# Optimization experiments

Hardware: AMD Instinct MI355X
Metric: run time of the kernel (lower is better)

## Reference

```python
import jax, jax.numpy as jnp
import numpy as np

N, E, D, G = 100000, 600000, 128, 256  # nodes, edges, feat dim, num graphs
EPS = 1e-5


def graph_norm(x, batch, weight, bias, mean_scale):
    # PyG GraphNorm: per-graph mean/var with learnable mean_scale
    counts = jax.ops.segment_sum(jnp.ones((x.shape[0],), x.dtype), batch, num_segments=G)
    counts = jnp.maximum(counts, 1.0)[:, None]  # [G,1]
    mean = jax.ops.segment_sum(x, batch, num_segments=G) / counts  # [G,D]
    out = x - mean[batch] * mean_scale  # [N,D]
    var = jax.ops.segment_sum(out * out, batch, num_segments=G) / counts  # [G,D]
    inv_std = jax.lax.rsqrt(var + EPS)[batch]  # [N,D]
    return weight * out * inv_std + bias


def sage_conv_max(x, edge_index, w_l, b_l, w_r):
    # SAGEConv(aggr='max'): gather x[src], scatter-max into dst, then two linears
    src, dst = edge_index[0], edge_index[1]
    agg = jax.ops.segment_max(x[src], dst, num_segments=N)  # [N,D], -inf for empty
    agg = jnp.where(jnp.isfinite(agg), agg, 0.0)  # PyG fills empty segments with 0
    return agg @ w_l.T + b_l + x @ w_r.T


def setup_inputs() -> dict:
    key = jax.random.key(0)
    ks = jax.random.split(key, 6)
    x = jax.random.normal(ks[0], (N, D), dtype=jnp.float32)
    edge_index = jax.random.randint(ks[1], (2, E), 0, N, dtype=jnp.int64)
    batch = jnp.sort(jax.random.randint(ks[2], (N,), 0, G, dtype=jnp.int64))
    s = 1.0 / np.sqrt(D)
    return {
        "x": x,
        "edge_index": edge_index,
        "batch": batch,
        "n1_w": jnp.ones((D,), jnp.float32),
        "n1_b": jnp.zeros((D,), jnp.float32),
        "n1_ms": jnp.ones((D,), jnp.float32),
        "n2_w": jnp.ones((D,), jnp.float32),
        "n2_b": jnp.zeros((D,), jnp.float32),
        "n2_ms": jnp.ones((D,), jnp.float32),
        "w_l": jax.random.uniform(ks[3], (D, D), jnp.float32, -s, s),
        "b_l": jax.random.uniform(ks[4], (D,), jnp.float32, -s, s),
        "w_r": jax.random.uniform(ks[5], (D, D), jnp.float32, -s, s),
    }


def reference(x, edge_index, batch, n1_w, n1_b, n1_ms, n2_w, n2_b, n2_ms, w_l, b_l, w_r):
    h = graph_norm(x, batch, n1_w, n1_b, n1_ms)
    h = sage_conv_max(h, edge_index, w_l, b_l, w_r)
    h = jax.nn.relu(x + h)
    h = graph_norm(h, batch, n2_w, n2_b, n2_ms)
    return h
```

## Files before the change

kernel.cpp:

```cpp
#include <hip/hip_runtime.h>
#include <math.h>

#define NN 100000
#define EE 600000
#define DD 128
#define GG 256
#define EPSV 1e-5f

typedef __attribute__((ext_vector_type(8))) __bf16 bf16x8;
typedef __attribute__((ext_vector_type(16))) float f32x16;
typedef __attribute__((ext_vector_type(4))) unsigned short us4;

#define OFF_A1      0
#define OFF_B1      131072
#define OFF_A2      262144
#define OFF_B2      393216
#define OFF_DEG     524288
#define OFF_ROWPTR  924288
#define OFF_CURSOR  1324352
#define OFF_BSUMS   1724352
#define OFF_CNT     1726400
#define OFF_ELIST   1728448
#define OFF_WB      4128448
#define OFF_H1B     4193984
#define WS_NEED_A   (OFF_H1B + 25600000ULL)

#define NB_STATS 782
#define NB_EDGE  2344
#define NB_H1B   12500
#define NB1024   98

__device__ __forceinline__ int lower_bound_i(const int* __restrict__ a, int n, int v) {
    int lo = 0, hi = n;
    while (lo < hi) { int mid = (lo + hi) >> 1; if (a[mid] < v) lo = mid + 1; else hi = mid; }
    return lo;
}

__device__ __forceinline__ unsigned short f2bf(float f) {
    unsigned int u = __float_as_uint(f);
    unsigned int r = u + 0x7fffu + ((u >> 16) & 1u);
    return (unsigned short)(r >> 16);
}

__device__ __forceinline__ void stats_body(
    const float* __restrict__ X, const int* __restrict__ batch,
    float* __restrict__ Sg, float* __restrict__ Qg, int blk)
{
    int t = threadIdx.x;
    int rl = t >> 5, fq = t & 31;
    int r0 = blk * 128;
    int rend = r0 + 128; if (rend > NN) rend = NN;
    __shared__ float ls[8 * 128];
    __shared__ float lq[8 * 128];
    int g0 = batch[r0], g1 = batch[rend - 1];
    const float4* X4 = (const float4*)X;
    for (int g = g0; g <= g1; ++g) {
        int sa = (g == g0) ? r0   : lower_bound_i(batch, NN, g);
        int sb = (g == g1) ? rend : lower_bound_i(batch, NN, g + 1);
        float s0 = 0.f, s1 = 0.f, s2 = 0.f, s3 = 0.f;
        float q0 = 0.f, q1 = 0.f, q2 = 0.f, q3 = 0.f;
        for (int r = sa + rl; r < sb; r += 8) {
            float4 v = X4[r * 32 + fq];
            s0 += v.x; s1 += v.y; s2 += v.z; s3 += v.w;
            q0 += v.x * v.x; q1 += v.y * v.y; q2 += v.z * v.z; q3 += v.w * v.w;
        }
        ls[rl * 128 + fq * 4 + 0] = s0; ls[rl * 128 + fq * 4 + 1] = s1;
        ls[rl * 128 + fq * 4 + 2] = s2; ls[rl * 128 + fq * 4 + 3] = s3;
        lq[rl * 128 + fq * 4 + 0] = q0; lq[rl * 128 + fq * 4 + 1] = q1;
        lq[rl * 128 + fq * 4 + 2] = q2; lq[rl * 128 + fq * 4 + 3] = q3;
        __syncthreads();
        if (t < 32) {
            #pragma unroll
            for (int k = 0; k < 4; k++) {
                float as = 0.f, aq = 0.f;
                #pragma unroll
                for (int j = 0; j < 8; j++) { as += ls[j * 128 + t * 4 + k]; aq += lq[j * 128 + t * 4 + k]; }
                atomicAdd(&Sg[g * DD + t * 4 + k], as);
                atomicAdd(&Qg[g * DD + t * 4 + k], aq);
            }
        }
        __syncthreads();
    }
}

__global__ __launch_bounds__(256) void stats_p1(
    const float* __restrict__ X, const int* __restrict__ batch,
    float* __restrict__ Sg, float* __restrict__ Qg)
{
    stats_body(X, batch, Sg, Qg, blockIdx.x);
}

__global__ __launch_bounds__(256) void statsdeg_kernel(
    const float* __restrict__ X, const int* __restrict__ batch,
    float* __restrict__ Sg, float* __restrict__ Qg,
    const int* __restrict__ dst, int* __restrict__ deg)
{
    int b = blockIdx.x;
    if (b < NB_STATS) { stats_body(X, batch, Sg, Qg, b); return; }
    int e = (b - NB_STATS) * 256 + threadIdx.x;
    if (e < EE) atomicAdd(&deg[dst[e]], 1);
}

__global__ __launch_bounds__(128) void finalize_kernel(
    const int* __restrict__ batch, float* S, float* Q,
    const float* __restrict__ w, const float* __restrict__ bb, const float* __restrict__ ms,
    unsigned short* __restrict__ wb, const float* __restrict__ wl, const float* __restrict__ wr,
    int* __restrict__ cnt, int doW)
{
    int g = blockIdx.x;
    if (g >= GG) {
        if (!doW) return;
        const float* W = (g == GG) ? wl : wr;
        int kofs = (g == GG) ? 0 : 128;
        for (int tt = threadIdx.x; tt < DD * 32; tt += 128) {
            int j = tt >> 5, k4 = tt & 31;
            float4 v = ((const float4*)W)[j * 32 + k4];
            us4 o = { f2bf(v.x), f2bf(v.y), f2bf(v.z), f2bf(v.w) };
            *(us4*)&wb[j * 256 + kofs + k4 * 4] = o;
        }
        return;
    }
    __shared__ int sh[2];
    if (threadIdx.x == 0) { sh[0] = lower_bound_i(batch, NN, g); sh[1] = lower_bound_i(batch, NN, g + 1); }
    __syncthreads();
    int c_n = sh[1] - sh[0];
    if (cnt && threadIdx.x == 0) cnt[g] = c_n;
    float c = (float)(c_n > 0 ? c_n : 1);
    float inv_c = 1.0f / c;
    int d = threadIdx.x;
    float m  = S[g * DD + d] * inv_c;
    float qm = Q[g * DD + d] * inv_c;
    float sc = ms[d];
    float var = qm - m * m * sc * (2.0f - sc);
    float Ad = w[d] * rsqrtf(var + EPSV);
    S[g * DD + d] = Ad;
    Q[g * DD + d] = bb[d] - Ad * m * sc;
}

__global__ __launch_bounds__(256) void h1bscan_kernel(
    const float* __restrict__ X, const int* __restrict__ batch,
    const float* __restrict__ A1, const float* __restrict__ B1, unsigned short* __restrict__ h1b,
    const int* __restrict__ deg, int* __restrict__ bsums)
{
    int blk = blockIdx.x;
    if (blk < NB_H1B) {
        int f = blk * 256 + threadIdx.x;
        int i = f >> 5, c = f & 31;
        int g = batch[i];
        float4 v = ((const float4*)X)[f];
        float4 a = ((const float4*)A1)[g * 32 + c];
        float4 b = ((const float4*)B1)[g * 32 + c];
        us4 o = { f2bf(fmaf(a.x, v.x, b.x)), f2bf(fmaf(a.y, v.y, b.y)),
                  f2bf(fmaf(a.z, v.z, b.z)), f2bf(fmaf(a.w, v.w, b.w)) };
        *(us4*)&h1b[i * DD + c * 4] = o;
        return;
    }
    int b = blk - NB_H1B, t = threadIdx.x;
    int base = b * 1024 + t * 4;
    int v = 0;
    #pragma unroll
    for (int k = 0; k < 4; k++) { int i = base + k; if (i < NN) v += deg[i]; }
    __shared__ int sd[256];
    sd[t] = v; __syncthreads();
    for (int off = 128; off > 0; off >>= 1) { if (t < off) sd[t] += sd[t + off]; __syncthreads(); }
    if (t == 0) bsums[b] = sd[0];
}

__global__ __launch_bounds__(256) void scan1(const int* __restrict__ deg, int* __restrict__ bsums) {
    int b = blockIdx.x, t = threadIdx.x;
    int base = b * 1024 + t * 4;
    int v = 0;
    #pragma unroll
    for (int k = 0; k < 4; k++) { int i = base + k; if (i < NN) v += deg[i]; }
    __shared__ int sd[256];
    sd[t] = v; __syncthreads();
    for (int off = 128; off > 0; off >>= 1) { if (t < off) sd[t] += sd[t + off]; __syncthreads(); }
    if (t == 0) bsums[b] = sd[0];
}

__global__ __launch_bounds__(256) void scan3(const int* __restrict__ deg, const int* __restrict__ bsums,
                                             int* __restrict__ rowptr, int* __restrict__ cursor) {
    int b = blockIdx.x, t = threadIdx.x;
    int boff = 0;
    for (int j = 0; j < b; j++) boff += bsums[j];
    int base = b * 1024 + t * 4;
    int d0 = 0, d1 = 0, d2 = 0, d3 = 0;
    if (base     < NN) d0 = deg[base];
    if (base + 1 < NN) d1 = deg[base + 1];
    if (base + 2 < NN) d2 = deg[base + 2];
    if (base + 3 < NN) d3 = deg[base + 3];
    int tsum = d0 + d1 + d2 + d3;
    __shared__ int sd[256];
    sd[t] = tsum; __syncthreads();
    for (int off = 1; off < 256; off <<= 1) {
        int a = (t >= off) ? sd[t - off] : 0;
        __syncthreads();
        sd[t] += a;
        __syncthreads();
    }
    int exc = sd[t] - tsum + boff;
    int p0 = exc, p1 = exc + d0, p2 = exc + d0 + d1, p3 = exc + d0 + d1 + d2;
    if (base     < NN) { rowptr[base]     = p0; cursor[base]     = p0; }
    if (base + 1 < NN) { rowptr[base + 1] = p1; cursor[base + 1] = p1; }
    if (base + 2 < NN) { rowptr[base + 2] = p2; cursor[base + 2] = p2; }
    if (base + 3 < NN) { rowptr[base + 3] = p3; cursor[base + 3] = p3; }
    if (b == 0 && t == 0) rowptr[NN] = EE;
}

__global__ __launch_bounds__(256) void fill_kernel(const int* __restrict__ src, const int* __restrict__ dst,
                                                   int* __restrict__ cursor, int* __restrict__ elist) {
    int e = blockIdx.x * 256 + threadIdx.x;
    if (e < EE) {
        int p = atomicAdd(&cursor[dst[e]], 1);
        elist[p] = src[e];
    }
}

#define USTR 264
__global__ __launch_bounds__(512) void gemm_mega(
    const float* __restrict__ X, const unsigned short* __restrict__ h1b,
    const int* __restrict__ batch, const int* __restrict__ rowptr, const int* __restrict__ elist,
    const unsigned short* __restrict__ wb, const float* __restrict__ blv,
    float* __restrict__ Sg2, float* __restrict__ Qg2, float* __restrict__ out)
{
    __shared__ unsigned short sU[64 * USTR];
    __shared__ int sBatch[64];
    int tid = threadIdx.x;
    int i0 = blockIdx.x * 64;
    int lane = tid & 63, wave = tid >> 6;
    int m = lane & 31, hf = lane >> 5;

    for (int t = tid; t < 64 * 16; t += 512) {
        int r = t >> 4, c = t & 15;
        int i = i0 + r; if (i >= NN) i = NN - 1;
        uint4 v = ((const uint4*)(h1b + (size_t)i * DD))[c];
        *(uint4*)&sU[r * USTR + 128 + c * 8] = v;
    }
    if (tid < 64) {
        int i = i0 + tid;
        sBatch[tid] = (i < NN) ? batch[i] : -1;
    }

    int hw = tid >> 5, j = tid & 31;
    for (int rr = hw; rr < 64; rr += 16) {
        int i = i0 + rr;
        int beg = 0, end = 0;
        if (i < NN) { beg = rowptr[i]; end = rowptr[i + 1]; }
        float a0 = -INFINITY, a1 = -INFINITY, a2 = -INFINITY, a3 = -INFINITY;
        int last = end - 1;
        for (int e = beg; e < end; e += 8) {
            int n[8];
            #pragma unroll
            for (int k = 0; k < 8; k++) { int t2 = e + k; n[k] = elist[t2 < last ? t2 : last]; }
            us4 p[8];
            #pragma unroll
            for (int k = 0; k < 8; k++) p[k] = *(const us4*)(h1b + (size_t)n[k] * DD + j * 4);
            #pragma unroll
            for (int k = 0; k < 8; k++) {
                a0 = fmaxf(a0, __uint_as_float((unsigned)p[k][0] << 16));
                a1 = fmaxf(a1, __uint_as_float((unsigned)p[k][1] << 16));
                a2 = fmaxf(a2, __uint_as_float((unsigned)p[k][2] << 16));
                a3 = fmaxf(a3, __uint_as_float((unsigned)p[k][3] << 16));
            }
        }
        us4 r4 = { 0, 0, 0, 0 };
        if (end > beg) {
            r4[0] = (unsigned short)(__float_as_uint(a0) >> 16);
            r4[1] = (unsigned short)(__float_as_uint(a1) >> 16);
            r4[2] = (unsigned short)(__float_as_uint(a2) >> 16);
            r4[3] = (unsigned short)(__float_as_uint(a3) >> 16);
        }
        *(us4*)&sU[rr * USTR + j * 4] = r4;
    }
    __syncthreads();

    int rbase = (wave >> 2) * 32;
    int col = (wave & 3) * 32 + m;
    const unsigned short* bcol = wb + col * 256 + hf * 8;
    const unsigned short* arow = &sU[(rbase + m) * USTR + hf * 8];

    f32x16 acc;
    #pragma unroll
    for (int r = 0; r < 16; r++) acc[r] = 0.f;
    #pragma unroll
    for (int s = 0; s < 16; s++) {
        bf16x8 b = *(const bf16x8*)(bcol + s * 16);
        bf16x8 a = *(const bf16x8*)(arow + s * 16);
        acc = __builtin_amdgcn_mfma_f32_32x32x16_bf16(a, b, acc, 0, 0, 0);
    }

    float blc = blv[col];
    float s_run = 0.f, q_run = 0.f;
    int cur_g = -1;
    #pragma unroll
    for (int reg = 0; reg < 16; reg++) {
        int rl = (reg & 3) + 8 * (reg >> 2) + 4 * hf;
        int i = i0 + rbase + rl;
        if (i < NN) {
            float v = X[i * DD + col] + blc + acc[reg];
            v = v > 0.f ? v : 0.f;
            out[i * DD + col] = v;
            int g = sBatch[rbase + rl];
            if (g != cur_g) {
                if (cur_g >= 0) {
                    atomicAdd(&Sg2[cur_g * DD + col], s_run);
                    atomicAdd(&Qg2[cur_g * DD + col], q_run);
                }
                cur_g = g; s_run = 0.f; q_run = 0.f;
            }
            s_run += v; q_run += v * v;
        }
    }
    if (cur_g >= 0) {
        atomicAdd(&Sg2[cur_g * DD + col], s_run);
        atomicAdd(&Qg2[cur_g * DD + col], q_run);
    }
}

__global__ __launch_bounds__(256) void apply_a(
    float* __restrict__ H, const int* __restrict__ batch,
    const float* __restrict__ Sg2, const float* __restrict__ Qg2, const int* __restrict__ cnt,
    const float* __restrict__ w2, const float* __restrict__ b2, const float* __restrict__ ms2)
{
    int f = blockIdx.x * 256 + threadIdx.x;
    if (f >= NN * 32) return;
    int i = f >> 5, c = f & 31;
    int g = batch[i];
    int cg = cnt[g];
    float invc = 1.0f / (float)(cg > 0 ? cg : 1);
    float4 S  = ((const float4*)Sg2)[g * 32 + c];
    float4 Q  = ((const float4*)Qg2)[g * 32 + c];
    float4 W  = ((const float4*)w2)[c];
    float4 Bv = ((const float4*)b2)[c];
    float4 Ms = ((const float4*)ms2)[c];
    float4 v = ((float4*)H)[f];
    {
        float mm = S.x * invc, qm = Q.x * invc;
        float A = W.x * rsqrtf(qm - mm * mm * Ms.x * (2.0f - Ms.x) + EPSV);
        v.x = fmaf(A, v.x, Bv.x - A * mm * Ms.x);
    }
    {
        float mm = S.y * invc, qm = Q.y * invc;
        float A = W.y * rsqrtf(qm - mm * mm * Ms.y * (2.0f - Ms.y) + EPSV);
        v.y = fmaf(A, v.y, Bv.y - A * mm * Ms.y);
    }
    {
        float mm = S.z * invc, qm = Q.z * invc;
        float A = W.z * rsqrtf(qm - mm * mm * Ms.z * (2.0f - Ms.z) + EPSV);
        v.z = fmaf(A, v.z, Bv.z - A * mm * Ms.z);
    }
    {
        float mm = S.w * invc, qm = Q.w * invc;
        float A = W.w * rsqrtf(qm - mm * mm * Ms.w * (2.0f - Ms.w) + EPSV);
        v.w = fmaf(A, v.w, Bv.w - A * mm * Ms.w);
    }
    ((float4*)H)[f] = v;
}

__global__ __launch_bounds__(256) void apply_b(float* __restrict__ H, const int* __restrict__ batch,
                                               const float* __restrict__ A2, const float* __restrict__ B2) {
    int f = blockIdx.x * 256 + threadIdx.x;
    if (f >= NN * 32) return;
    int i = f >> 5, c = f & 31;
    int g = batch[i];
    float4 v = ((float4*)H)[f];
    float4 a = ((const float4*)A2)[g * 32 + c];
    float4 b = ((const float4*)B2)[g * 32 + c];
    v.x = fmaf(a.x, v.x, b.x); v.y = fmaf(a.y, v.y, b.y);
    v.z = fmaf(a.z, v.z, b.z); v.w = fmaf(a.w, v.w, b.w);
    ((float4*)H)[f] = v;
}

__global__ __launch_bounds__(256) void agg_b(
    const float* __restrict__ X, const int* __restrict__ batch,
    const float* __restrict__ A1, const float* __restrict__ B1,
    const int* __restrict__ rowptr, const int* __restrict__ elist, float* __restrict__ H)
{
    int i = blockIdx.x * 2 + (threadIdx.x >> 7);
    int d = threadIdx.x & 127;
    int beg = rowptr[i], end = rowptr[i + 1];
    float acc = -INFINITY;
    int e = beg;
    for (; e + 2 <= end; e += 2) {
        int s0 = elist[e], s1 = elist[e + 1];
        int g0 = batch[s0], g1 = batch[s1];
        float v0 = fmaf(A1[g0 * DD + d], X[s0 * DD + d], B1[g0 * DD + d]);
        float v1 = fmaf(A1[g1 * DD + d], X[s1 * DD + d], B1[g1 * DD + d]);
        acc = fmaxf(acc, fmaxf(v0, v1));
    }
    for (; e < end; e++) {
        int s = elist[e]; int g = batch[s];
        acc = fmaxf(acc, fmaf(A1[g * DD + d], X[s * DD + d], B1[g * DD + d]));
    }
    if (end == beg) acc = 0.f;
    H[i * DD + d] = acc;
}

#define BM 128
#define LDT 72
__global__ __launch_bounds__(256) void gemm_b(
    const float* __restrict__ X, const int* __restrict__ batch,
    const float* __restrict__ A1, const float* __restrict__ B1,
    const float* __restrict__ wl, const float* __restrict__ blv, const float* __restrict__ wr,
    float* __restrict__ H)
{
    __shared__ unsigned short Ut[BM * LDT];
    __shared__ unsigned short Wt[DD * LDT];
    int i0 = blockIdx.x * BM;
    int tid = threadIdx.x;
    int lane = tid & 63, wave = tid >> 6;
    int wrow = (wave >> 1) * 64, wcol = (wave & 1) * 64;
    int m = lane & 31, hf = lane >> 5;

    f32x16 acc00, acc01, acc10, acc11;
    #pragma unroll
    for (int r = 0; r < 16; r++) { acc00[r] = 0.f; acc01[r] = 0.f; acc10[r] = 0.f; acc11[r] = 0.f; }

    for (int c = 0; c < 4; c++) {
        __syncthreads();
        for (int t = tid; t < BM * 16; t += 256) {
            int r = t >> 4, c4 = t & 15;
            int i = i0 + r; if (i >= NN) i = NN - 1;
            float4 v;
            if (c < 2) {
                v = ((const float4*)H)[i * 32 + c * 16 + c4];
            } else {
                int g = batch[i];
                float4 xv = ((const float4*)X)[i * 32 + (c - 2) * 16 + c4];
                float4 a = ((const float4*)A1)[g * 32 + (c - 2) * 16 + c4];
                float4 b = ((const float4*)B1)[g * 32 + (c - 2) * 16 + c4];
                v.x = fmaf(a.x, xv.x, b.x); v.y = fmaf(a.y, xv.y, b.y);
                v.z = fmaf(a.z, xv.z, b.z); v.w = fmaf(a.w, xv.w, b.w);
            }
            us4 o = { f2bf(v.x), f2bf(v.y), f2bf(v.z), f2bf(v.w) };
            *(us4*)&Ut[r * LDT + c4 * 4] = o;
        }
        {
            const float* Wsrc = (c < 2) ? wl : wr;
            int kb = (c & 1) * 16;
            for (int t = tid; t < DD * 16; t += 256) {
                int j = t >> 4, c4 = t & 15;
                float4 v = ((const float4*)Wsrc)[j * 32 + kb + c4];
                us4 o = { f2bf(v.x), f2bf(v.y), f2bf(v.z), f2bf(v.w) };
                *(us4*)&Wt[j * LDT + c4 * 4] = o;
            }
        }
        __syncthreads();
        #pragma unroll
        for (int kk = 0; kk < 4; kk++) {
            int kb2 = kk * 16 + hf * 8;
            bf16x8 a0 = *(const bf16x8*)&Ut[(wrow      + m) * LDT + kb2];
            bf16x8 a1 = *(const bf16x8*)&Ut[(wrow + 32 + m) * LDT + kb2];
            bf16x8 b0 = *(const bf16x8*)&Wt[(wcol      + m) * LDT + kb2];
            bf16x8 b1 = *(const bf16x8*)&Wt[(wcol + 32 + m) * LDT + kb2];
            acc00 = __builtin_amdgcn_mfma_f32_32x32x16_bf16(a0, b0, acc00, 0, 0, 0);
            acc01 = __builtin_amdgcn_mfma_f32_32x32x16_bf16(a0, b1, acc01, 0, 0, 0);
            acc10 = __builtin_amdgcn_mfma_f32_32x32x16_bf16(a1, b0, acc10, 0, 0, 0);
            acc11 = __builtin_amdgcn_mfma_f32_32x32x16_bf16(a1, b1, acc11, 0, 0, 0);
        }
    }

    int col0 = wcol + m, col1 = wcol + 32 + m;
    float bl0 = blv[col0], bl1 = blv[col1];
    #pragma unroll
    for (int reg = 0; reg < 16; reg++) {
        int rl = (reg & 3) + 8 * (reg >> 2) + 4 * hf;
        int ia = i0 + wrow + rl;
        int ib = i0 + wrow + 32 + rl;
        if (ia < NN) {
            float v0 = X[ia * DD + col0] + bl0 + acc00[reg];
            float v1 = X[ia * DD + col1] + bl1 + acc01[reg];
            H[ia * DD + col0] = v0 > 0.f ? v0 : 0.f;
            H[ia * DD + col1] = v1 > 0.f ? v1 : 0.f;
        }
        if (ib < NN) {
            float v0 = X[ib * DD + col0] + bl0 + acc10[reg];
            float v1 = X[ib * DD + col1] + bl1 + acc11[reg];
            H[ib * DD + col0] = v0 > 0.f ? v0 : 0.f;
            H[ib * DD + col1] = v1 > 0.f ? v1 : 0.f;
        }
    }
}

extern "C" void kernel_launch(void* const* d_in, const int* in_sizes, int n_in,
                              void* d_out, int out_size, void* d_ws, size_t ws_size,
                              hipStream_t stream) {
    const float* x    = (const float*)d_in[0];
    const int*   ei   = (const int*)d_in[1];
    const int*   batch= (const int*)d_in[2];
    const float* n1w  = (const float*)d_in[3];
    const float* n1b  = (const float*)d_in[4];
    const float* n1ms = (const float*)d_in[5];
    const float* n2w  = (const float*)d_in[6];
    const float* n2b  = (const float*)d_in[7];
    const float* n2ms = (const float*)d_in[8];
    const float* wl   = (const float*)d_in[9];
    const float* bl   = (const float*)d_in[10];
    const float* wr   = (const float*)d_in[11];
    float* out = (float*)d_out;

    char* w = (char*)d_ws;
    float* A1     = (float*)(w + OFF_A1);
    float* B1     = (float*)(w + OFF_B1);
    float* A2     = (float*)(w + OFF_A2);
    float* B2     = (float*)(w + OFF_B2);
    int*   deg    = (int*)(w + OFF_DEG);
    int*   rowptr = (int*)(w + OFF_ROWPTR);
    int*   cursor = (int*)(w + OFF_CURSOR);
    int*   bsums  = (int*)(w + OFF_BSUMS);
    int*   cnt    = (int*)(w + OFF_CNT);
    int*   elist  = (int*)(w + OFF_ELIST);
    unsigned short* wb  = (unsigned short*)(w + OFF_WB);
    unsigned short* h1b = (unsigned short*)(w + OFF_H1B);

    const int* src = ei;
    const int* dst = ei + EE;
    bool bigws = (ws_size >= WS_NEED_A);

    hipMemsetAsync(w, 0, OFF_ROWPTR, stream);

    statsdeg_kernel<<<NB_STATS + NB_EDGE, 256, 0, stream>>>(x, batch, A1, B1, dst, deg);
    finalize_kernel<<<GG + 2, 128, 0, stream>>>(batch, A1, B1, n1w, n1b, n1ms,
                                                wb, wl, wr, cnt, bigws ? 1 : 0);

    if (bigws) {
        h1bscan_kernel<<<NB_H1B + NB1024, 256, 0, stream>>>(x, batch, A1, B1, h1b, deg, bsums);
        scan3<<<NB1024, 256, 0, stream>>>(deg, bsums, rowptr, cursor);
        fill_kernel<<<NB_EDGE, 256, 0, stream>>>(src, dst, cursor, elist);

        gemm_mega<<<(NN + 63) / 64, 512, 0, stream>>>(x, h1b, batch, rowptr, elist,
                                                      wb, bl, A2, B2, out);

        apply_a<<<NB_H1B, 256, 0, stream>>>(out, batch, A2, B2, cnt, n2w, n2b, n2ms);
    } else {
        scan1<<<NB1024, 256, 0, stream>>>(deg, bsums);
        scan3<<<NB1024, 256, 0, stream>>>(deg, bsums, rowptr, cursor);
        fill_kernel<<<NB_EDGE, 256, 0, stream>>>(src, dst, cursor, elist);

        agg_b<<<NN / 2, 256, 0, stream>>>(x, batch, A1, B1, rowptr, elist, out);
        gemm_b<<<(NN + BM - 1) / BM, 256, 0, stream>>>(x, batch, A1, B1, wl, bl, wr, out);

        stats_p1<<<NB_STATS, 256, 0, stream>>>(out, batch, A2, B2);
        finalize_kernel<<<GG, 128, 0, stream>>>(batch, A2, B2, n2w, n2b, n2ms,
                                                (unsigned short*)nullptr,
                                                (const float*)nullptr, (const float*)nullptr,
                                                (int*)nullptr, 0);
        apply_b<<<NB_H1B, 256, 0, stream>>>(out, batch, A2, B2);
    }
}
```

Baseline: 300.2 us.

## Make fused aggregate-GEMM kernel persistent with atomic tile queue and LDS edge staging

The fused aggregation plus GEMM kernel now launches a fixed grid of 1024 blocks. Each block repeatedly takes 64-row tiles from a global atomic counter, which is reset in fill_kernel. Per tile, the row pointers and up to 1280 edge-list entries are staged into shared memory before the max-gather, with a global-memory fallback for tiles that have more edges. This aims to even out load imbalance from varying node degrees, cut block launch overhead, and replace scattered global elist reads with LDS reads. In exchange it adds an atomic per tile, extra barriers, and more shared memory per block, which may lower occupancy.

```diff
diff --git a/kernel.cpp b/kernel.cpp
--- a/kernel.cpp
+++ b/kernel.cpp
@@ -20,6 +20,7 @@
 #define OFF_CURSOR  1324352
 #define OFF_BSUMS   1724352
 #define OFF_CNT     1726400
+#define OFF_CTR     1727424
 #define OFF_ELIST   1728448
 #define OFF_WB      4128448
 #define OFF_H1B     4193984
@@ -29,6 +30,8 @@
 #define NB_EDGE  2344
 #define NB_H1B   12500
 #define NB1024   98
+#define NTILES   1563
+#define SE_CAP   1280
 
 __device__ __forceinline__ int lower_bound_i(const int* __restrict__ a, int n, int v) {
     int lo = 0, hi = n;
@@ -208,7 +211,9 @@
 }
 
 __global__ __launch_bounds__(256) void fill_kernel(const int* __restrict__ src, const int* __restrict__ dst,
-                                                   int* __restrict__ cursor, int* __restrict__ elist) {
+                                                   int* __restrict__ cursor, int* __restrict__ elist,
+                                                   int* __restrict__ ctr) {
+    if (blockIdx.x == 0 && threadIdx.x == 0) ctr[0] = 0;
     int e = blockIdx.x * 256 + threadIdx.x;
     if (e < EE) {
         int p = atomicAdd(&cursor[dst[e]], 1);
@@ -221,99 +226,136 @@
     const float* __restrict__ X, const unsigned short* __restrict__ h1b,
     const int* __restrict__ batch, const int* __restrict__ rowptr, const int* __restrict__ elist,
     const unsigned short* __restrict__ wb, const float* __restrict__ blv,
-    float* __restrict__ Sg2, float* __restrict__ Qg2, float* __restrict__ out)
+    float* __restrict__ Sg2, float* __restrict__ Qg2, float* __restrict__ out,
+    int* __restrict__ ctr)
 {
     __shared__ unsigned short sU[64 * USTR];
     __shared__ int sBatch[64];
+    __shared__ int sRP[65];
+    __shared__ int sE[SE_CAP];
+    __shared__ int sTile;
     int tid = threadIdx.x;
-    int i0 = blockIdx.x * 64;
     int lane = tid & 63, wave = tid >> 6;
     int m = lane & 31, hf = lane >> 5;
 
-    for (int t = tid; t < 64 * 16; t += 512) {
-        int r = t >> 4, c = t & 15;
-        int i = i0 + r; if (i >= NN) i = NN - 1;
-        uint4 v = ((const uint4*)(h1b + (size_t)i * DD))[c];
-        *(uint4*)&sU[r * USTR + 128 + c * 8] = v;
-    }
-    if (tid < 64) {
-        int i = i0 + tid;
-        sBatch[tid] = (i < NN) ? batch[i] : -1;
-    }
-
-    int hw = tid >> 5, j = tid & 31;
-    for (int rr = hw; rr < 64; rr += 16) {
-        int i = i0 + rr;
-        int beg = 0, end = 0;
-        if (i < NN) { beg = rowptr[i]; end = rowptr[i + 1]; }
-        float a0 = -INFINITY, a1 = -INFINITY, a2 = -INFINITY, a3 = -INFINITY;
-        int last = end - 1;
-        for (int e = beg; e < end; e += 8) {
-            int n[8];
-            #pragma unroll
-            for (int k = 0; k < 8; k++) { int t2 = e + k; n[k] = elist[t2 < last ? t2 : last]; }
-            us4 p[8];
-            #pragma unroll
-            for (int k = 0; k < 8; k++) p[k] = *(const us4*)(h1b + (size_t)n[k] * DD + j * 4);
-            #pragma unroll
-            for (int k = 0; k < 8; k++) {
-                a0 = fmaxf(a0, __uint_as_float((unsigned)p[k][0] << 16));
-                a1 = fmaxf(a1, __uint_as_float((unsigned)p[k][1] << 16));
-                a2 = fmaxf(a2, __uint_as_float((unsigned)p[k][2] << 16));
-                a3 = fmaxf(a3, __uint_as_float((unsigned)p[k][3] << 16));
+    for (;;) {
+        if (tid == 0) sTile = atomicAdd(ctr, 1);
+        __syncthreads();
+        int tile = sTile;
+        if (tile >= NTILES) return;
+        int i0 = tile * 64;
+
+        if (tid < 65) { int i = i0 + tid; sRP[tid] = rowptr[i < NN ? i : NN]; }
+        if (tid < 64) { int i = i0 + tid; sBatch[tid] = (i < NN) ? batch[i] : -1; }
+
+        for (int t = tid; t < 64 * 16; t += 512) {
+            int r = t >> 4, c = t & 15;
+            int i = i0 + r; if (i >= NN) i = NN - 1;
+            uint4 v = ((const uint4*)(h1b + (size_t)i * DD))[c];
+            *(uint4*)&sU[r * USTR + 128 + c * 8] = v;
+        }
+        __syncthreads();
+
+        int rp0 = sRP[0];
+        int L = sRP[64] - rp0;
+        int Lc = L < SE_CAP ? L : SE_CAP;
+        for (int t = tid; t < Lc; t += 512) sE[t] = elist[rp0 + t];
+        __syncthreads();
+
+        int hw = tid >> 5, j = tid & 31;
+        for (int rr = hw; rr < 64; rr += 16) {
+            int beg = sRP[rr] - rp0;
+            int end = sRP[rr + 1] - rp0;
+            float a0 = -INFINITY, a1 = -INFINITY, a2 = -INFINITY, a3 = -INFINITY;
+            int last = end - 1;
+            if (last < SE_CAP) {
+                for (int e = beg; e < end; e += 8) {
+                    int n[8];
+                    #pragma unroll
+                    for (int k = 0; k < 8; k++) { int t2 = e + k; n[k] = sE[t2 < last ? t2 : last]; }
+                    us4 p[8];
+                    #pragma unroll
+                    for (int k = 0; k < 8; k++) p[k] = *(const us4*)(h1b + (size_t)n[k] * DD + j * 4);
+                    #pragma unroll
+                    for (int k = 0; k < 8; k++) {
+                        a0 = fmaxf(a0, __uint_as_float((unsigned)p[k][0] << 16));
+                        a1 = fmaxf(a1, __uint_as_float((unsigned)p[k][1] << 16));
+                        a2 = fmaxf(a2, __uint_as_float((unsigned)p[k][2] << 16));
+                        a3 = fmaxf(a3, __uint_as_float((unsigned)p[k][3] << 16));
+                    }
+                }
+            } else {
+                for (int e = beg; e < end; e += 8) {
+                    int n[8];
+                    #pragma unroll
+                    for (int k = 0; k < 8; k++) {
+                        int t2 = e + k; if (t2 > last) t2 = last;
+                        n[k] = (t2 < SE_CAP) ? sE[t2] : elist[rp0 + t2];
+                    }
+                    us4 p[8];
+                    #pragma unroll
+                    for (int k = 0; k < 8; k++) p[k] = *(const us4*)(h1b + (size_t)n[k] * DD + j * 4);
+                    #pragma unroll
+                    for (int k = 0; k < 8; k++) {
+                        a0 = fmaxf(a0, __uint_as_float((unsigned)p[k][0] << 16));
+                        a1 = fmaxf(a1, __uint_as_float((unsigned)p[k][1] << 16));
+                        a2 = fmaxf(a2, __uint_as_float((unsigned)p[k][2] << 16));
+                        a3 = fmaxf(a3, __uint_as_float((unsigned)p[k][3] << 16));
+                    }
+                }
             }
-        }
-        us4 r4 = { 0, 0, 0, 0 };
-        if (end > beg) {
-            r4[0] = (unsigned short)(__float_as_uint(a0) >> 16);
-            r4[1] = (unsigned short)(__float_as_uint(a1) >> 16);
-            r4[2] = (unsigned short)(__float_as_uint(a2) >> 16);
-            r4[3] = (unsigned short)(__float_as_uint(a3) >> 16);
-        }
-        *(us4*)&sU[rr * USTR + j * 4] = r4;
-    }
-    __syncthreads();
-
-    int rbase = (wave >> 2) * 32;
-    int col = (wave & 3) * 32 + m;
-    const unsigned short* bcol = wb + col * 256 + hf * 8;
-    const unsigned short* arow = &sU[(rbase + m) * USTR + hf * 8];
-
-    f32x16 acc;
-    #pragma unroll
-    for (int r = 0; r < 16; r++) acc[r] = 0.f;
-    #pragma unroll
-    for (int s = 0; s < 16; s++) {
-        bf16x8 b = *(const bf16x8*)(bcol + s * 16);
-        bf16x8 a = *(const bf16x8*)(arow + s * 16);
-        acc = __builtin_amdgcn_mfma_f32_32x32x16_bf16(a, b, acc, 0, 0, 0);
-    }
-
-    float blc = blv[col];
-    float s_run = 0.f, q_run = 0.f;
-    int cur_g = -1;
-    #pragma unroll
-    for (int reg = 0; reg < 16; reg++) {
-        int rl = (reg & 3) + 8 * (reg >> 2) + 4 * hf;
-        int i = i0 + rbase + rl;
-        if (i < NN) {
-            float v = X[i * DD + col] + blc + acc[reg];
-            v = v > 0.f ? v : 0.f;
-            out[i * DD + col] = v;
-            int g = sBatch[rbase + rl];
-            if (g != cur_g) {
-                if (cur_g >= 0) {
-                    atomicAdd(&Sg2[cur_g * DD + col], s_run);
-                    atomicAdd(&Qg2[cur_g * DD + col], q_run);
+            us4 r4 = { 0, 0, 0, 0 };
+            if (end > beg) {
+                r4[0] = (unsigned short)(__float_as_uint(a0) >> 16);
+                r4[1] = (unsigned short)(__float_as_uint(a1) >> 16);
+                r4[2] = (unsigned short)(__float_as_uint(a2) >> 16);
+                r4[3] = (unsigned short)(__float_as_uint(a3) >> 16);
+            }
+            *(us4*)&sU[rr * USTR + j * 4] = r4;
+        }
+        __syncthreads();
+
+        int rbase = (wave >> 2) * 32;
+        int col = (wave & 3) * 32 + m;
+        const unsigned short* bcol = wb + col * 256 + hf * 8;
+        const unsigned short* arow = &sU[(rbase + m) * USTR + hf * 8];
+
+        f32x16 acc;
+        #pragma unroll
+        for (int r = 0; r < 16; r++) acc[r] = 0.f;
+        #pragma unroll
+        for (int s = 0; s < 16; s++) {
+            bf16x8 b = *(const bf16x8*)(bcol + s * 16);
+            bf16x8 a = *(const bf16x8*)(arow + s * 16);
+            acc = __builtin_amdgcn_mfma_f32_32x32x16_bf16(a, b, acc, 0, 0, 0);
+        }
+
+        float blc = blv[col];
+        float s_run = 0.f, q_run = 0.f;
+        int cur_g = -1;
+        #pragma unroll
+        for (int reg = 0; reg < 16; reg++) {
+            int rl = (reg & 3) + 8 * (reg >> 2) + 4 * hf;
+            int i = i0 + rbase + rl;
+            if (i < NN) {
+                float v = X[i * DD + col] + blc + acc[reg];
+                v = v > 0.f ? v : 0.f;
+                out[i * DD + col] = v;
+                int g = sBatch[rbase + rl];
+                if (g != cur_g) {
+                    if (cur_g >= 0) {
+                        atomicAdd(&Sg2[cur_g * DD + col], s_run);
+                        atomicAdd(&Qg2[cur_g * DD + col], q_run);
+                    }
+                    cur_g = g; s_run = 0.f; q_run = 0.f;
                 }
-                cur_g = g; s_run = 0.f; q_run = 0.f;
+                s_run += v; q_run += v * v;
             }
-            s_run += v; q_run += v * v;
-        }
-    }
-    if (cur_g >= 0) {
-        atomicAdd(&Sg2[cur_g * DD + col], s_run);
-        atomicAdd(&Qg2[cur_g * DD + col], q_run);
+        }
+        if (cur_g >= 0) {
+            atomicAdd(&Sg2[cur_g * DD + col], s_run);
+            atomicAdd(&Qg2[cur_g * DD + col], q_run);
+        }
     }
 }
 
@@ -509,6 +551,7 @@
     int*   cursor = (int*)(w + OFF_CURSOR);
     int*   bsums  = (int*)(w + OFF_BSUMS);
     int*   cnt    = (int*)(w + OFF_CNT);
+    int*   ctr    = (int*)(w + OFF_CTR);
     int*   elist  = (int*)(w + OFF_ELIST);
     unsigned short* wb  = (unsigned short*)(w + OFF_WB);
     unsigned short* h1b = (unsigned short*)(w + OFF_H1B);
@@ -526,16 +569,16 @@
     if (bigws) {
         h1bscan_kernel<<<NB_H1B + NB1024, 256, 0, stream>>>(x, batch, A1, B1, h1b, deg, bsums);
         scan3<<<NB1024, 256, 0, stream>>>(deg, bsums, rowptr, cursor);
-        fill_kernel<<<NB_EDGE, 256, 0, stream>>>(src, dst, cursor, elist);
-
-        gemm_mega<<<(NN + 63) / 64, 512, 0, stream>>>(x, h1b, batch, rowptr, elist,
-                                                      wb, bl, A2, B2, out);
+        fill_kernel<<<NB_EDGE, 256, 0, stream>>>(src, dst, cursor, elist, ctr);
+
+        gemm_mega<<<1024, 512, 0, stream>>>(x, h1b, batch, rowptr, elist,
+                                            wb, bl, A2, B2, out, ctr);
 
         apply_a<<<NB_H1B, 256, 0, stream>>>(out, batch, A2, B2, cnt, n2w, n2b, n2ms);
     } else {
         scan1<<<NB1024, 256, 0, stream>>>(deg, bsums);
         scan3<<<NB1024, 256, 0, stream>>>(deg, bsums, rowptr, cursor);
-        fill_kernel<<<NB_EDGE, 256, 0, stream>>>(src, dst, cursor, elist);
+        fill_kernel<<<NB_EDGE, 256, 0, stream>>>(src, dst, cursor, elist, ctr);
 
         agg_b<<<NN / 2, 256, 0, stream>>>(x, batch, A1, B1, rowptr, elist, out);
         gemm_b<<<(NN + BM - 1) / BM, 256, 0, stream>>>(x, batch, A1, B1, wl, bl, wr, out);
```

Measured after the change: 304.9 us. No clear change (+1.6%).
